# Optimization experiments

Hardware: AMD Instinct MI355X
Metric: run time of the kernel (lower is better)

## Reference

```python
import jax, jax.numpy as jnp
import numpy as np

B, C, H, W = 8, 512, 96, 96
CQ = C // 4


def setup_inputs() -> dict:
    key = jax.random.key(0)
    ks = jax.random.split(key, 8)
    s = 1.0 / np.sqrt(C)
    return {
        "x": jax.random.normal(ks[0], (B, C, H, W), jnp.float32),
        "Wq": jax.random.normal(ks[1], (CQ, C), jnp.float32) * s,
        "bq": jax.random.normal(ks[2], (CQ,), jnp.float32) * 0.01,
        "Wk": jax.random.normal(ks[3], (CQ, C), jnp.float32) * s,
        "bk": jax.random.normal(ks[4], (CQ,), jnp.float32) * 0.01,
        "Wv": jax.random.normal(ks[5], (C, C), jnp.float32) * s,
        "bv": jax.random.normal(ks[6], (C,), jnp.float32) * 0.01,
        "gamma": jax.random.normal(ks[7], (1,), jnp.float32) * 0.1,
    }


def _conv1x1(x, Wt, b):
    # 1x1 conv == per-pixel channel matmul: [B,C,H,W] x [O,C] -> [B,O,H,W]
    return jnp.einsum("bchw,oc->bohw", x, Wt) + b[None, :, None, None]


def reference(x, Wq, bq, Wk, bk, Wv, bv, gamma):
    b, c, h, w = x.shape
    q = _conv1x1(x, Wq, bq)  # [B,CQ,H,W]
    k = _conv1x1(x, Wk, bk)  # [B,CQ,H,W]
    v = _conv1x1(x, Wv, bv)  # [B,C ,H,W]

    # column (height-axis) attention energies, diagonal masked to -inf
    energy_H = jnp.einsum("bchw,bcjw->bhwj", q, k)  # [B,H,W,H]
    diag = jnp.eye(h, dtype=bool)[:, None, :]  # [H,1,H] broadcast over W
    energy_H = jnp.where(diag[None], -jnp.inf, energy_H)
    # row (width-axis) attention energies
    energy_W = jnp.einsum("bchw,bchj->bhwj", q, k)  # [B,H,W,W]

    att = jax.nn.softmax(jnp.concatenate([energy_H, energy_W], axis=3), axis=3)
    att_H = att[..., :h]       # [B,H,W,H]
    att_W = att[..., h:h + w]  # [B,H,W,W]

    out_H = jnp.einsum("bcjw,bhwj->bchw", v, att_H)
    out_W = jnp.einsum("bchj,bhwj->bchw", v, att_W)
    return gamma[0] * (out_H + out_W) + x
```

## Files before the change

kernel.cpp:

```cpp
#include <hip/hip_runtime.h>


#define B_ 8
#define C_ 512
#define CQ_ 128
#define H_ 96
#define W_ 96
#define HW_ 9216
#define J_ 192

typedef __attribute__((ext_vector_type(8))) short short8;
typedef __attribute__((ext_vector_type(4))) float f32x4;

__device__ __forceinline__ unsigned short f2bf(float f) {
    unsigned u = __float_as_uint(f);
    u += 0x7FFFu + ((u >> 16) & 1u);
    return (unsigned short)(u >> 16);
}
__device__ __forceinline__ float bf2f(unsigned short h) {
    return __uint_as_float((unsigned)h << 16);
}
__device__ __forceinline__ unsigned short f2h(float f) {
    _Float16 h = (_Float16)f;
    return __builtin_bit_cast(unsigned short, h);
}
__device__ __forceinline__ float h2f(unsigned short u) {
    return (float)__builtin_bit_cast(_Float16, u);
}
__device__ __forceinline__ void gl_lds16(const unsigned short* g, void* lds_base) {
    __builtin_amdgcn_global_load_lds((const __attribute__((address_space(1))) void*)g,
                                     (__attribute__((address_space(3))) void*)lds_base,
                                     16, 0, 0);
}

__global__ __launch_bounds__(256) void k0_wconv(const float* __restrict__ Wq,
                                                const float* __restrict__ Wk,
                                                const float* __restrict__ Wv,
                                                unsigned short* __restrict__ Wqk,
                                                unsigned short* __restrict__ Wvb) {
    int i = blockIdx.x * 256 + threadIdx.x;
    if (i < 65536)        Wqk[i] = f2bf(Wq[i]);
    else if (i < 131072)  Wqk[i] = f2bf(Wk[i - 65536]);
    else                  Wvb[i - 131072] = f2bf(Wv[i - 131072]);
}

__global__ __launch_bounds__(256) void k1_xT(const float* __restrict__ x,
                                             unsigned short* __restrict__ xT,
                                             unsigned short* __restrict__ xP) {
    __shared__ unsigned short t[32][33];
    int b = blockIdx.z, c0 = blockIdx.y * 32, p0 = blockIdx.x * 32;
    int tx = threadIdx.x, ty = threadIdx.y;
    const float* xb = x + (size_t)b * C_ * HW_;
    #pragma unroll
    for (int k = 0; k < 4; ++k) {
        int c = c0 + ty + k * 8;
        unsigned short v = f2bf(xb[(size_t)c * HW_ + p0 + tx]);
        t[ty + k * 8][tx] = v;
        xP[((size_t)b * C_ + c) * HW_ + p0 + tx] = v;
    }
    __syncthreads();
    unsigned short* xTb = xT + (size_t)b * HW_ * C_;
    #pragma unroll
    for (int k = 0; k < 4; ++k) {
        int p = p0 + ty + k * 8;
        xTb[(size_t)p * C_ + c0 + tx] = t[tx][ty + k * 8];
    }
}

__global__ __launch_bounds__(256) void k3_vt(const unsigned short* __restrict__ src_,
                                             unsigned short* __restrict__ dst_) {
    __shared__ unsigned short tl[96][97];
    int plane = blockIdx.x;
    const unsigned short* src = src_ + (size_t)plane * HW_;
    unsigned short* dst = dst_ + (size_t)plane * HW_;
    for (int e = threadIdx.x; e < HW_; e += 256) tl[e / 96][e % 96] = src[e];
    __syncthreads();
    for (int e = threadIdx.x; e < HW_; e += 256) { int w = e / 96, h = e % 96; dst[e] = tl[h][w]; }
}

__global__ __launch_bounds__(512) void k2a_qk(const unsigned short* __restrict__ xT,
                                              const unsigned short* __restrict__ Wqk,
                                              const float* __restrict__ bq,
                                              const float* __restrict__ bk,
                                              unsigned short* __restrict__ Qb,
                                              unsigned short* __restrict__ Kb) {
    __shared__ alignas(16) unsigned short As[128][64];
    __shared__ alignas(16) unsigned short Bs[256][64];
    int t = threadIdx.x;
    int p0 = blockIdx.x * 128;
    int wid = t >> 6, lane = t & 63;
    int wr = wid >> 2, wc = wid & 3;
    int srow = lane >> 3;
    int sk8 = (((lane & 7) ^ srow) << 3);
    const f32x4 zero = {0.f, 0.f, 0.f, 0.f};
    f32x4 acc[4][4];
    for (int m = 0; m < 4; ++m) for (int n = 0; n < 4; ++n) acc[m][n] = zero;
    for (int ks = 0; ks < 512; ks += 64) {
        #pragma unroll
        for (int i = 0; i < 2; ++i) {
            int q = wid * 2 + i; int row = q * 8 + srow;
            gl_lds16(xT + ((size_t)(p0 + row) << 9) + ks + sk8, (char*)&As[0][0] + q * 1024);
        }
        #pragma unroll
        for (int i = 0; i < 4; ++i) {
            int q = wid * 4 + i; int row = q * 8 + srow;
            gl_lds16(Wqk + ((size_t)row << 9) + ks + sk8, (char*)&Bs[0][0] + q * 1024);
        }
        __syncthreads();
        #pragma unroll
        for (int kk = 0; kk < 2; ++kk) {
            int po = (((kk * 4 + (lane >> 4)) ^ (lane & 7)) << 3);
            short8 af[4], bfv[4];
            #pragma unroll
            for (int m = 0; m < 4; ++m) af[m] = *(const short8*)(&As[wr * 64 + m * 16 + (lane & 15)][po]);
            #pragma unroll
            for (int n = 0; n < 4; ++n) bfv[n] = *(const short8*)(&Bs[wc * 64 + n * 16 + (lane & 15)][po]);
            #pragma unroll
            for (int m = 0; m < 4; ++m)
                #pragma unroll
                for (int n = 0; n < 4; ++n)
                    acc[m][n] = __builtin_amdgcn_mfma_f32_16x16x32_bf16(af[m], bfv[n], acc[m][n], 0, 0, 0);
        }
        __syncthreads();
    }
    #pragma unroll
    for (int n = 0; n < 4; ++n) {
        int oc = wc * 64 + n * 16 + (lane & 15);
        float bias = (oc < 128) ? bq[oc] : bk[oc - 128];
        unsigned short* dst = (oc < 128) ? (Qb + oc) : (Kb + (oc - 128));
        #pragma unroll
        for (int m = 0; m < 4; ++m) {
            int pr = p0 + wr * 64 + m * 16 + ((lane >> 4) << 2);
            #pragma unroll
            for (int r = 0; r < 4; ++r)
                dst[(size_t)(pr + r) << 7] = f2bf(acc[m][n][r] + bias);
        }
    }
}

__global__ __launch_bounds__(256) void k4_energy(const unsigned short* __restrict__ Qb,
                                                 const unsigned short* __restrict__ Kb,
                                                 unsigned short* __restrict__ att) {
    __shared__ alignas(16) unsigned short Qs[96][136];
    __shared__ alignas(16) unsigned short Ks[96][136];
    int t = threadIdx.x;
    int modeH = blockIdx.z;
    int b = blockIdx.y, v0 = blockIdx.x;
    size_t base, rstride, obase_off, ostride;
    if (!modeH) {
        base      = (size_t)((b * H_ + v0) * W_) * CQ_;
        rstride   = CQ_;
        obase_off = (size_t)((b * H_ + v0) * W_) * J_ + H_;
        ostride   = J_;
    } else {
        base      = ((size_t)(b * H_) * W_ + v0) * CQ_;
        rstride   = (size_t)W_ * CQ_;
        obase_off = ((size_t)(b * H_) * W_ + v0) * J_;
        ostride   = (size_t)W_ * J_;
    }
    for (int q = t; q < 1536; q += 256) {
        int row = q >> 4, c8 = (q & 15) << 3;
        *(uint4*)(&Qs[row][c8]) = *(const uint4*)(Qb + base + (size_t)row * rstride + c8);
        *(uint4*)(&Ks[row][c8]) = *(const uint4*)(Kb + base + (size_t)row * rstride + c8);
    }
    __syncthreads();
    int wid = t >> 6, lane = t & 63;
    int wr = wid >> 1, wc = wid & 1;
    const f32x4 zero = {0.f, 0.f, 0.f, 0.f};
    f32x4 acc[3][3];
    for (int m = 0; m < 3; ++m) for (int n = 0; n < 3; ++n) acc[m][n] = zero;
    #pragma unroll
    for (int ks = 0; ks < 128; ks += 32) {
        int ko = ks + ((lane >> 4) << 3);
        short8 af[3], bfv[3];
        #pragma unroll
        for (int m = 0; m < 3; ++m) af[m] = *(const short8*)(&Qs[wr * 48 + m * 16 + (lane & 15)][ko]);
        #pragma unroll
        for (int n = 0; n < 3; ++n) bfv[n] = *(const short8*)(&Ks[wc * 48 + n * 16 + (lane & 15)][ko]);
        #pragma unroll
        for (int m = 0; m < 3; ++m)
            #pragma unroll
            for (int n = 0; n < 3; ++n)
                acc[m][n] = __builtin_amdgcn_mfma_f32_16x16x32_bf16(af[m], bfv[n], acc[m][n], 0, 0, 0);
    }
    unsigned short* ob = att + obase_off;
    #pragma unroll
    for (int m = 0; m < 3; ++m) {
        int i = wr * 48 + m * 16 + ((lane >> 4) << 2);
        #pragma unroll
        for (int n = 0; n < 3; ++n) {
            int j = wc * 48 + n * 16 + (lane & 15);
            #pragma unroll
            for (int r = 0; r < 4; ++r) {
                float v = acc[m][n][r];
                if (modeH && (i + r) == j) v = -__builtin_inff();
                ob[(size_t)(i + r) * ostride + j] = f2h(v);
            }
        }
    }
}

__global__ __launch_bounds__(256) void k5_softmax(const unsigned short* __restrict__ att,
                                                  unsigned short* __restrict__ att2) {
    int r = blockIdx.x * 4 + (threadIdx.x >> 6);
    int lane = threadIdx.x & 63;
    const unsigned short* row = att + (size_t)r * J_;
    float e0 = h2f(row[lane]), e1 = h2f(row[lane + 64]), e2 = h2f(row[lane + 128]);
    float m = fmaxf(e0, fmaxf(e1, e2));
    #pragma unroll
    for (int off = 32; off; off >>= 1) m = fmaxf(m, __shfl_xor(m, off, 64));
    float p0 = __expf(e0 - m), p1 = __expf(e1 - m), p2 = __expf(e2 - m);
    float s = p0 + p1 + p2;
    #pragma unroll
    for (int off = 32; off; off >>= 1) s += __shfl_xor(s, off, 64);
    float inv = 1.f / s;
    unsigned short* orow = att2 + (size_t)r * J_;
    orow[lane]       = f2bf(p0 * inv);
    orow[lane + 64]  = f2bf(p1 * inv);
    orow[lane + 128] = f2bf(p2 * inv);
}

template <int MODE>
__global__ __launch_bounds__(512) void k6_agg(const unsigned short* __restrict__ att2,
                                              const unsigned short* __restrict__ Xsrc,
                                              unsigned short* __restrict__ xAgg) {
    __shared__ alignas(16) unsigned short As[96][104];
    __shared__ alignas(16) unsigned short Bs[256][104];
    int t = threadIdx.x;
    int c0 = blockIdx.x * 256;
    int b = blockIdx.y / 96;
    int v = blockIdx.y % 96;
    size_t abase, astride;
    if (MODE == 0) { abase = ((size_t)(b * HW_) + (size_t)v * 96) * J_ + 96; astride = J_; }
    else           { abase = (size_t)(b * HW_) * J_ + (size_t)v * J_;        astride = (size_t)96 * J_; }
    if (t < 192) {
        int row = t >> 1, cs = (t & 1) * 6;
        const unsigned short* src = att2 + abase + (size_t)row * astride;
        #pragma unroll
        for (int i = 0; i < 6; ++i)
            *(uint4*)(&As[row][(cs + i) * 8]) = *(const uint4*)(src + (cs + i) * 8);
    }
    {
        int row = t >> 1, cs = (t & 1) * 6;
        const unsigned short* src = Xsrc + ((size_t)(b * C_) + c0 + row) * HW_ + v * 96;
        #pragma unroll
        for (int i = 0; i < 6; ++i)
            *(uint4*)(&Bs[row][(cs + i) * 8]) = *(const uint4*)(src + (cs + i) * 8);
    }
    __syncthreads();
    int wid = t >> 6, lane = t & 63;
    int wr = wid >> 2, wc = wid & 3;
    const f32x4 zero = {0.f, 0.f, 0.f, 0.f};
    f32x4 acc[3][4];
    for (int m = 0; m < 3; ++m) for (int n = 0; n < 4; ++n) acc[m][n] = zero;
    #pragma unroll
    for (int ks = 0; ks < 96; ks += 32) {
        int ko = ks + ((lane >> 4) << 3);
        short8 af[3], bfv[4];
        #pragma unroll
        for (int m = 0; m < 3; ++m) af[m] = *(const short8*)(&As[wr * 48 + m * 16 + (lane & 15)][ko]);
        #pragma unroll
        for (int n = 0; n < 4; ++n) bfv[n] = *(const short8*)(&Bs[wc * 64 + n * 16 + (lane & 15)][ko]);
        #pragma unroll
        for (int m = 0; m < 3; ++m)
            #pragma unroll
            for (int n = 0; n < 4; ++n)
                acc[m][n] = __builtin_amdgcn_mfma_f32_16x16x32_bf16(af[m], bfv[n], acc[m][n], 0, 0, 0);
    }
    #pragma unroll
    for (int m = 0; m < 3; ++m) {
        int orow = wr * 48 + m * 16 + ((lane >> 4) << 2);
        #pragma unroll
        for (int n = 0; n < 4; ++n) {
            int c = c0 + wc * 64 + n * 16 + (lane & 15);
            #pragma unroll
            for (int r = 0; r < 4; ++r) {
                int p = (MODE == 0) ? (v * 96 + orow + r) : ((orow + r) * 96 + v);
                size_t o = ((size_t)(b * HW_) + p) * C_ + c;
                if (MODE == 0) xAgg[o] = f2bf(acc[m][n][r]);
                else           xAgg[o] = f2bf(bf2f(xAgg[o]) + acc[m][n][r]);
            }
        }
    }
}

__global__ __launch_bounds__(256) void k9_proj(const unsigned short* __restrict__ xAgg,
                                               const unsigned short* __restrict__ Wvb,
                                               const float* __restrict__ bv,
                                               const unsigned short* __restrict__ xPb,
                                               const float* __restrict__ gamma_p,
                                               float* __restrict__ outp) {
    __shared__ alignas(16) char smem[32768];
    unsigned short* AsBase = (unsigned short*)smem;
    unsigned short* BsBase = (unsigned short*)(smem + 16384);
    int t = threadIdx.x;
    int bid = blockIdx.x;
    int tile = (bid & 7) * 288 + (bid >> 3);
    int oc0 = (tile & 3) * 128;
    int pt  = tile >> 2;
    int p0  = pt * 128;
    int wid = t >> 6, lane = t & 63;
    int wr = wid >> 1, wc = wid & 1;
    int srow = lane >> 2;
    int sk8 = (((lane & 3) ^ (srow & 3)) << 3);
    const f32x4 zero = {0.f, 0.f, 0.f, 0.f};
    f32x4 acc[4][4];
    for (int m = 0; m < 4; ++m) for (int n = 0; n < 4; ++n) acc[m][n] = zero;

    auto STAGE = [&](int buf, int ks) {
        #pragma unroll
        for (int i = 0; i < 2; ++i) {
            int q = wid * 2 + i; int row = q * 16 + srow;
            gl_lds16(Wvb + ((size_t)(oc0 + row) << 9) + ks + sk8,
                     smem + buf * 8192 + q * 1024);
        }
        #pragma unroll
        for (int i = 0; i < 2; ++i) {
            int q = wid * 2 + i; int row = q * 16 + srow;
            gl_lds16(xAgg + ((size_t)(p0 + row) << 9) + ks + sk8,
                     smem + 16384 + buf * 8192 + q * 1024);
        }
    };

    STAGE(0, 0);
    #pragma unroll
    for (int step = 0; step < 16; ++step) {
        int cur = step & 1;
        if (step < 15) {
            STAGE(cur ^ 1, (step + 1) * 32);
            asm volatile("s_waitcnt vmcnt(4)" ::: "memory");
        } else {
            asm volatile("s_waitcnt vmcnt(0)" ::: "memory");
        }
        __builtin_amdgcn_s_barrier();
        __builtin_amdgcn_sched_barrier(0);
        {
            short8 af[4], bfv[4];
            #pragma unroll
            for (int m = 0; m < 4; ++m) {
                int row = wr * 64 + m * 16 + (lane & 15);
                int po = (((lane >> 4) ^ (row & 3)) << 3);
                af[m] = *(const short8*)(AsBase + cur * 4096 + row * 32 + po);
            }
            #pragma unroll
            for (int n = 0; n < 4; ++n) {
                int row = wc * 64 + n * 16 + (lane & 15);
                int po = (((lane >> 4) ^ (row & 3)) << 3);
                bfv[n] = *(const short8*)(BsBase + cur * 4096 + row * 32 + po);
            }
            #pragma unroll
            for (int m = 0; m < 4; ++m)
                #pragma unroll
                for (int n = 0; n < 4; ++n)
                    acc[m][n] = __builtin_amdgcn_mfma_f32_16x16x32_bf16(af[m], bfv[n], acc[m][n], 0, 0, 0);
        }
        __builtin_amdgcn_s_barrier();
    }
    __syncthreads();

    #pragma unroll
    for (int m = 0; m < 4; ++m) {
        int rowb = wr * 64 + m * 16 + ((lane >> 4) << 2);
        #pragma unroll
        for (int r = 0; r < 4; ++r) {
            int row = rowb + r;
            float bias = bv[oc0 + row];
            #pragma unroll
            for (int n = 0; n < 4; ++n) {
                int col = wc * 64 + n * 16 + (lane & 15);
                int baddr = row * 256 + ((col << 1) ^ ((row & 7) << 4));
                *(unsigned short*)(smem + baddr) = f2bf(acc[m][n][r] + bias);
            }
        }
    }
    __syncthreads();

    int b = pt / 72;
    int hw0 = (pt % 72) * 128;
    float g = gamma_p[0];
    #pragma unroll
    for (int pass = 0; pass < 16; ++pass) {
        int row = pass * 8 + (t >> 5);
        int cs = (t & 31) * 4;
        uint2 tv = *(const uint2*)(smem + row * 256 + ((cs << 1) ^ ((row & 7) << 4)));
        int oc = oc0 + row;
        size_t o = ((size_t)(b * C_ + oc)) * HW_ + hw0 + cs;
        uint2 xv = *(const uint2*)(xPb + o);
        f32x4 ov;
        ov[0] = g * bf2f((unsigned short)(tv.x & 0xFFFF)) + bf2f((unsigned short)(xv.x & 0xFFFF));
        ov[1] = g * bf2f((unsigned short)(tv.x >> 16))    + bf2f((unsigned short)(xv.x >> 16));
        ov[2] = g * bf2f((unsigned short)(tv.y & 0xFFFF)) + bf2f((unsigned short)(xv.y & 0xFFFF));
        ov[3] = g * bf2f((unsigned short)(tv.y >> 16))    + bf2f((unsigned short)(xv.y >> 16));
        *(f32x4*)(outp + o) = ov;
    }
}

extern "C" void kernel_launch(void* const* d_in, const int* in_sizes, int n_in,
                              void* d_out, int out_size, void* d_ws, size_t ws_size,
                              hipStream_t stream) {
    const float* x  = (const float*)d_in[0];
    const float* Wq = (const float*)d_in[1];
    const float* bq = (const float*)d_in[2];
    const float* Wk = (const float*)d_in[3];
    const float* bk = (const float*)d_in[4];
    const float* Wv = (const float*)d_in[5];
    const float* bv = (const float*)d_in[6];
    const float* gm = (const float*)d_in[7];
    float* out = (float*)d_out;
    char* ws = (char*)d_ws;

    unsigned short* xT    = (unsigned short*)(ws + 0);
    unsigned short* xAgg  = (unsigned short*)(ws + 0);
    unsigned short* xP    = (unsigned short*)(ws + 75497472);
    unsigned short* Qb    = (unsigned short*)(ws + 150994944);
    unsigned short* att2  = (unsigned short*)(ws + 150994944);
    unsigned short* Kb    = (unsigned short*)(ws + 169869312);
    unsigned short* Wqk   = (unsigned short*)(ws + 188743680);
    unsigned short* Wvb   = (unsigned short*)(ws + 189005824);
    unsigned short* attf  = (unsigned short*)d_out;
    unsigned short* xPT   = (unsigned short*)((char*)d_out + 75497472);

    k0_wconv<<<1536, 256, 0, stream>>>(Wq, Wk, Wv, Wqk, Wvb);
    k1_xT<<<dim3(288, 16, 8), dim3(32, 8, 1), 0, stream>>>(x, xT, xP);
    k2a_qk<<<576, 512, 0, stream>>>(xT, Wqk, bq, bk, Qb, Kb);
    k3_vt<<<4096, 256, 0, stream>>>(xP, xPT);
    k4_energy<<<dim3(96, 8, 2), 256, 0, stream>>>(Qb, Kb, attf);
    k5_softmax<<<18432, 256, 0, stream>>>(attf, att2);
    k6_agg<0><<<dim3(2, 768), 512, 0, stream>>>(att2, xP, xAgg);
    k6_agg<1><<<dim3(2, 768), 512, 0, stream>>>(att2, xPT, xAgg);
    k9_proj<<<2304, 256, 0, stream>>>(xAgg, Wvb, bv, xP, gm, out);
}
```

Baseline: 370.4 us.

## Double-buffer LDS staging in Q/K projection GEMM with async prefetch

Restructures the k2a_qk GEMM main loop to use two LDS buffers with K-step 32. The next tile's global-to-LDS loads are issued before computing on the current tile, with explicit vmcnt waits and raw barriers. This overlaps memory latency with MFMA work in this kernel. The cost is a changed swizzle and finer K steps, which means more barriers, and only this one of several kernels is affected.

After: 364.0 us. About the same (-1.7%).

```diff
diff --git a/kernel.cpp b/kernel.cpp
--- a/kernel.cpp
+++ b/kernel.cpp
@@ -84,44 +84,66 @@
                                               const float* __restrict__ bk,
                                               unsigned short* __restrict__ Qb,
                                               unsigned short* __restrict__ Kb) {
-    __shared__ alignas(16) unsigned short As[128][64];
-    __shared__ alignas(16) unsigned short Bs[256][64];
+    __shared__ alignas(16) char smem[49152];
+    unsigned short* AsBase = (unsigned short*)smem;
+    unsigned short* BsBase = (unsigned short*)(smem + 16384);
     int t = threadIdx.x;
     int p0 = blockIdx.x * 128;
     int wid = t >> 6, lane = t & 63;
     int wr = wid >> 2, wc = wid & 3;
-    int srow = lane >> 3;
-    int sk8 = (((lane & 7) ^ srow) << 3);
+    int srow = lane >> 2;
+    int sk8 = (((lane & 3) ^ (srow & 3)) << 3);
     const f32x4 zero = {0.f, 0.f, 0.f, 0.f};
     f32x4 acc[4][4];
     for (int m = 0; m < 4; ++m) for (int n = 0; n < 4; ++n) acc[m][n] = zero;
-    for (int ks = 0; ks < 512; ks += 64) {
+
+    auto STAGE = [&](int buf, int ks) {
+        {
+            int q = wid; int row = q * 16 + srow;
+            gl_lds16(xT + ((size_t)(p0 + row) << 9) + ks + sk8,
+                     smem + buf * 8192 + q * 1024);
+        }
         #pragma unroll
         for (int i = 0; i < 2; ++i) {
-            int q = wid * 2 + i; int row = q * 8 + srow;
-            gl_lds16(xT + ((size_t)(p0 + row) << 9) + ks + sk8, (char*)&As[0][0] + q * 1024);
-        }
-        #pragma unroll
-        for (int i = 0; i < 4; ++i) {
-            int q = wid * 4 + i; int row = q * 8 + srow;
-            gl_lds16(Wqk + ((size_t)row << 9) + ks + sk8, (char*)&Bs[0][0] + q * 1024);
-        }
-        __syncthreads();
-        #pragma unroll
-        for (int kk = 0; kk < 2; ++kk) {
-            int po = (((kk * 4 + (lane >> 4)) ^ (lane & 7)) << 3);
+            int q = wid * 2 + i; int row = q * 16 + srow;
+            gl_lds16(Wqk + ((size_t)row << 9) + ks + sk8,
+                     smem + 16384 + buf * 16384 + q * 1024);
+        }
+    };
+
+    STAGE(0, 0);
+    #pragma unroll
+    for (int step = 0; step < 16; ++step) {
+        int cur = step & 1;
+        if (step < 15) {
+            STAGE(cur ^ 1, (step + 1) * 32);
+            asm volatile("s_waitcnt vmcnt(3)" ::: "memory");
+        } else {
+            asm volatile("s_waitcnt vmcnt(0)" ::: "memory");
+        }
+        __builtin_amdgcn_s_barrier();
+        __builtin_amdgcn_sched_barrier(0);
+        {
             short8 af[4], bfv[4];
             #pragma unroll
-            for (int m = 0; m < 4; ++m) af[m] = *(const short8*)(&As[wr * 64 + m * 16 + (lane & 15)][po]);
-            #pragma unroll
-            for (int n = 0; n < 4; ++n) bfv[n] = *(const short8*)(&Bs[wc * 64 + n * 16 + (lane & 15)][po]);
+            for (int m = 0; m < 4; ++m) {
+                int row = wr * 64 + m * 16 + (lane & 15);
+                int po = (((lane >> 4) ^ (row & 3)) << 3);
+                af[m] = *(const short8*)(AsBase + cur * 4096 + row * 32 + po);
+            }
+            #pragma unroll
+            for (int n = 0; n < 4; ++n) {
+                int row = wc * 64 + n * 16 + (lane & 15);
+                int po = (((lane >> 4) ^ (row & 3)) << 3);
+                bfv[n] = *(const short8*)(BsBase + cur * 8192 + row * 32 + po);
+            }
             #pragma unroll
             for (int m = 0; m < 4; ++m)
                 #pragma unroll
                 for (int n = 0; n < 4; ++n)
                     acc[m][n] = __builtin_amdgcn_mfma_f32_16x16x32_bf16(af[m], bfv[n], acc[m][n], 0, 0, 0);
         }
-        __syncthreads();
+        __builtin_amdgcn_s_barrier();
     }
     #pragma unroll
     for (int n = 0; n < 4; ++n) {
```
